# Kernel tuning notes

Hardware: AMD Instinct MI355X
Metric: run time of the kernel (lower is better)

Reference implementation:

```python
import jax, jax.numpy as jnp
import numpy as np

B, NS, NT, C = 32, 1000, 100, 256
LAMBDA_GIOU, LAMBDA_L1 = 10.0, 1.0


def _lsa(cost):
    """Hungarian / Jonker-Volgenant shortest-augmenting-path (numpy, O(n^2 m)).
    Matches scipy.optimize.linear_sum_assignment for rectangular matrices."""
    cost = np.asarray(cost, dtype=np.float64)
    transposed = cost.shape[0] > cost.shape[1]
    if transposed:
        cost = cost.T
    n, m = cost.shape  # n <= m
    INF = np.inf
    u = np.zeros(n + 1)
    v = np.zeros(m + 1)
    p = np.zeros(m + 1, dtype=np.int64)   # p[j] = row (1-based) assigned to col j
    way = np.zeros(m + 1, dtype=np.int64)
    for i in range(1, n + 1):
        p[0] = i
        j0 = 0
        minv = np.full(m + 1, INF)
        used = np.zeros(m + 1, dtype=bool)
        while True:
            used[j0] = True
            i0 = p[j0]
            cur = cost[i0 - 1, :] - u[i0] - v[1:]
            free = ~used[1:]
            better = free & (cur < minv[1:])
            minv[1:][better] = cur[better]
            way[1:][better] = j0
            masked = np.where(free, minv[1:], INF)
            j1 = int(np.argmin(masked)) + 1
            delta = masked[j1 - 1]
            u[p[used]] += delta
            v[used] -= delta
            minv[~used] -= delta
            j0 = j1
            if p[j0] == 0:
                break
        while j0:
            j1 = way[j0]
            p[j0] = p[j1]
            j0 = j1
    rows = p[1:] - 1
    cols = np.arange(m)
    keep = rows >= 0
    rows, cols = rows[keep], cols[keep]
    if transposed:
        rows, cols = cols, rows
    order = np.argsort(rows)
    return rows[order], cols[order]


def _pairwise_cost(logits, classes, sb, tb):
    """Per-batch (Ns,Nt) cost = CE(logits_s, class_t) + 10*(1-GIoU(box_s, box_t)) + L1mean."""
    Bc, Ns, Cd = logits.shape
    Nt = classes.shape[1]
    # Cross entropy: logsumexp over classes minus logit at target class (identical
    # math to the torch expand+flatten CE, without the Ns*Nt*C copy).
    lse = jax.nn.logsumexp(logits, axis=-1)  # (B,Ns)
    picked = jnp.take_along_axis(
        logits, jnp.broadcast_to(classes[:, None, :], (Bc, Ns, Nt)), axis=2)  # (B,Ns,Nt)
    ce = lse[:, :, None] - picked
    # Pairwise GIoU (boxes in xyxy)
    s = sb[:, :, None, :]  # (B,Ns,1,4)
    t = tb[:, None, :, :]  # (B,1,Nt,4)
    ix1 = jnp.maximum(s[..., 0], t[..., 0])
    iy1 = jnp.maximum(s[..., 1], t[..., 1])
    ix2 = jnp.minimum(s[..., 2], t[..., 2])
    iy2 = jnp.minimum(s[..., 3], t[..., 3])
    inter = jnp.clip(ix2 - ix1, 0.0) * jnp.clip(iy2 - iy1, 0.0)
    area_s = (s[..., 2] - s[..., 0]) * (s[..., 3] - s[..., 1])
    area_t = (t[..., 2] - t[..., 0]) * (t[..., 3] - t[..., 1])
    union = area_s + area_t - inter
    iou = inter / union
    cx1 = jnp.minimum(s[..., 0], t[..., 0])
    cy1 = jnp.minimum(s[..., 1], t[..., 1])
    cx2 = jnp.maximum(s[..., 2], t[..., 2])
    cy2 = jnp.maximum(s[..., 3], t[..., 3])
    carea = (cx2 - cx1) * (cy2 - cy1)
    giou = iou - (carea - union) / carea
    l1 = jnp.abs(s - t).mean(axis=-1)  # (B,Ns,Nt)
    return ce + LAMBDA_GIOU * (1.0 - giou) + LAMBDA_L1 * l1


def _valid_boxes(key, b, n):
    p = jax.random.uniform(key, (b, n, 2, 2), dtype=jnp.float32)
    lo = p.min(axis=2)
    hi = p.max(axis=2)
    return jnp.concatenate([lo, hi], axis=-1)  # (b,n,4) xyxy, x1<x2, y1<y2


def setup_inputs() -> dict:
    key = jax.random.key(0)
    k1, k2, k3, k4 = jax.random.split(key, 4)
    return {
        "source_class_logits": jax.random.normal(k1, (B, NS, C), dtype=jnp.float32),
        "target_classes": jax.random.randint(k2, (B, NT), 0, C, dtype=jnp.int32),
        "source_boxes": _valid_boxes(k3, B, NS),
        "target_boxes": _valid_boxes(k4, B, NT),
    }


def reference(source_class_logits, target_classes, source_boxes, target_boxes):
    cost = _pairwise_cost(source_class_logits, target_classes, source_boxes, target_boxes)
    cost_np = np.asarray(cost)
    rows_l, cols_l = [], []
    for b in range(cost_np.shape[0]):  # assignment is inherently per-matrix / host-side
        r, c = _lsa(cost_np[b])
        rows_l.append(r)
        cols_l.append(c)
    rows = jnp.asarray(np.stack(rows_l))  # (B, min(Ns,Nt))
    cols = jnp.asarray(np.stack(cols_l))
    bidx = jnp.arange(cost.shape[0])[:, None]
    return cost[bidx, rows, cols].mean(axis=1)  # (B,)
```

## Files before the change

kernel.cpp:

```cpp
#include <hip/hip_runtime.h>
#include <math.h>

#define NSRC 1000
#define NTGT 100
#define NCLS 256
#define NB   32
#define NSP  1024
#define CHUNK 64
#define NCHK  16
#define CEP   101
#define PAD_IDX(j) ((j) + ((j) >> 4))
#define LDSN (NSP + (NSP >> 4))
#define AUCTION_EPS 0.04f
#define NWAVES 8
#define ROUND_CAP 96


__global__ __launch_bounds__(512) void cost_kernel(const float* __restrict__ logits,
                                                   const int*   __restrict__ tcls,
                                                   const float* __restrict__ sbox,
                                                   const float* __restrict__ tbox,
                                                   float*       __restrict__ cost,
                                                   float*       __restrict__ pm1,
                                                   float*       __restrict__ pm2,
                                                   int*         __restrict__ pmi) {
    int b     = blockIdx.x & 31;
    int chunk = blockIdx.x >> 5;
    int s0    = chunk * CHUNK;
    int wid   = threadIdx.x >> 6;
    int lane  = threadIdx.x & 63;

    __shared__ float  ce_lds[CHUNK][CEP];
    __shared__ float4 sb_lds[CHUNK];
    __shared__ float4 tb_lds[NTGT];
    __shared__ int    cls_lds[128];

    for (int t = threadIdx.x; t < NTGT; t += 512) {
        tb_lds[t]  = reinterpret_cast<const float4*>(tbox)[b * NTGT + t];
        cls_lds[t] = tcls[b * NTGT + t];
    }
    if (threadIdx.x < 128 - NTGT) cls_lds[NTGT + threadIdx.x] = 0;
    int valid = NSRC - s0; valid = valid > CHUNK ? CHUNK : valid;
    for (int r = threadIdx.x; r < valid; r += 512)
        sb_lds[r] = reinterpret_cast<const float4*>(sbox)[b * NSRC + s0 + r];
    __syncthreads();

    int c0 = cls_lds[lane];
    int l0 = c0 >> 2, e0 = c0 & 3;
    int c1 = cls_lds[64 + lane];
    int l1s = c1 >> 2, e1 = c1 & 3;
    bool w1 = lane < NTGT - 64;
    #pragma unroll 4
    for (int r = wid; r < valid; r += 8) {
        int gs = b * NSRC + s0 + r;
        float4 v4 = reinterpret_cast<const float4*>(logits + (size_t)gs * NCLS)[lane];
        float m = fmaxf(fmaxf(v4.x, v4.y), fmaxf(v4.z, v4.w));
        #pragma unroll
        for (int off = 32; off >= 1; off >>= 1) m = fmaxf(m, __shfl_xor(m, off));
        float s = expf(v4.x - m) + expf(v4.y - m) + expf(v4.z - m) + expf(v4.w - m);
        #pragma unroll
        for (int off = 32; off >= 1; off >>= 1) s += __shfl_xor(s, off);
        float lse = m + logf(s);
        float px = __shfl(v4.x, l0), py = __shfl(v4.y, l0),
              pz = __shfl(v4.z, l0), pw = __shfl(v4.w, l0);
        float p0 = e0 == 0 ? px : e0 == 1 ? py : e0 == 2 ? pz : pw;
        ce_lds[r][lane] = lse - p0;
        float qx = __shfl(v4.x, l1s), qy = __shfl(v4.y, l1s),
              qz = __shfl(v4.z, l1s), qw = __shfl(v4.w, l1s);
        float p1 = e1 == 0 ? qx : e1 == 1 ? qy : e1 == 2 ? qz : qw;
        if (w1) ce_lds[r][64 + lane] = lse - p1;
    }
    __syncthreads();

    bool vs = lane < valid;
    float4 sb = sb_lds[vs ? lane : 0];
    float area_s = (sb.z - sb.x) * (sb.w - sb.y);
    int sg = s0 + lane;
    #pragma unroll 2
    for (int t = wid; t < NTGT; t += 8) {
        float4 tb = tb_lds[t];
        float area_t = (tb.z - tb.x) * (tb.w - tb.y);
        float c = 1e30f;
        if (vs) {
            float ce = ce_lds[lane][t];
            float ix1 = fmaxf(sb.x, tb.x), iy1 = fmaxf(sb.y, tb.y);
            float ix2 = fminf(sb.z, tb.z), iy2 = fminf(sb.w, tb.w);
            float inter = fmaxf(ix2 - ix1, 0.f) * fmaxf(iy2 - iy1, 0.f);
            float uni = area_s + area_t - inter;
            float iou = inter / uni;
            float cx1 = fminf(sb.x, tb.x), cy1 = fminf(sb.y, tb.y);
            float cx2 = fmaxf(sb.z, tb.z), cy2 = fmaxf(sb.w, tb.w);
            float carea = (cx2 - cx1) * (cy2 - cy1);
            float giou = iou - (carea - uni) / carea;
            float l1 = 0.25f * (fabsf(sb.x - tb.x) + fabsf(sb.y - tb.y) +
                                fabsf(sb.z - tb.z) + fabsf(sb.w - tb.w));
            c = ce + 10.0f * (1.0f - giou) + l1;
        }
        cost[(size_t)(b * NTGT + t) * NSP + sg] = c;
        float m1 = vs ? c : 1e38f, m2 = 1e38f;
        int   mi = vs ? sg : 0x7fffffff;
        #pragma unroll
        for (int off = 32; off >= 1; off >>= 1) {
            float om1 = __shfl_xor(m1, off);
            float om2 = __shfl_xor(m2, off);
            int   oi  = __shfl_xor(mi, off);
            bool take = (om1 < m1) || (om1 == m1 && oi < mi);
            float lose = take ? m1 : om1;
            m1 = take ? om1 : m1;
            mi = take ? oi  : mi;
            m2 = fminf(fminf(m2, om2), lose);
        }
        if (lane == 0) {
            int idx = (b * NTGT + t) * NCHK + chunk;
            pm1[idx] = m1; pm2[idx] = m2; pmi[idx] = mi;
        }
    }
}

__global__ __launch_bounds__(512) void lsa_kernel(const float* __restrict__ cost,
                                                  const float* __restrict__ pm1,
                                                  const float* __restrict__ pm2,
                                                  const int*   __restrict__ pmi,
                                                  float* __restrict__ out) {
    int b    = blockIdx.x;
    int tid  = threadIdx.x;
    int wv   = tid >> 6;
    int lane = tid & 63;
    const float* C = cost + (size_t)b * NTGT * NSP;
    __shared__ int   way[LDSN];
    __shared__ int   pcol[LDSN];
    __shared__ float uu[LDSN];
    __shared__ float vsh[LDSN];
    __shared__ float urow[NTGT];
    __shared__ int   done[NTGT];
    __shared__ float bm1[NTGT];
    __shared__ float bm2[NTGT];
    __shared__ int   bj [NTGT];
    __shared__ float bv [NTGT];
    __shared__ int   qbuf[1024];
    __shared__ int   qstate[2];
    __shared__ int   srow[NWAVES];

    for (int t = tid; t < LDSN; t += 512) {
        pcol[t] = -1; uu[t] = 0.f; vsh[t] = 0.f; way[t] = 0x7fffffff;
    }
    for (int t = tid; t < NTGT; t += 512) {
        int base16 = (b * NTGT + t) * NCHK;
        float m1 = pm1[base16], m2 = pm2[base16];
        int   mi = pmi[base16];
        #pragma unroll
        for (int k = 1; k < NCHK; ++k) {
            float om1 = pm1[base16 + k], om2 = pm2[base16 + k];
            int   oi  = pmi[base16 + k];
            bool take = (om1 < m1) || (om1 == m1 && oi < mi);
            float lose = take ? m1 : om1;
            m1 = take ? om1 : m1;
            mi = take ? oi  : mi;
            m2 = fminf(fminf(m2, om2), lose);
        }
        urow[t] = m1;
        bm1[t]  = m1;
        bm2[t]  = m2;
        bj[t]   = mi;
        bv[t]   = 0.f;
    }
    if (tid == 0) { qstate[0] = 0; qstate[1] = 0; }
    __syncthreads();

    for (int r = tid; r < NTGT; r += 512) atomicMin(&way[PAD_IDX(bj[r])], r);
    __syncthreads();
    for (int r = tid; r < NTGT; r += 512) {
        int j = bj[r];
        int w = (way[PAD_IDX(j)] == r) ? 1 : 0;
        done[r] = w;
        if (w) { pcol[PAD_IDX(j)] = r; uu[PAD_IDX(j)] = urow[r]; }
    }
    __syncthreads();

    if (tid < 64) {
        int qt = 0;
        #pragma unroll
        for (int r0 = 0; r0 < 128; r0 += 64) {
            int r = r0 + lane;
            bool act = (r < NTGT) && !done[r];
            unsigned long long mask = __ballot(act);
            if (act) qbuf[qt + __popcll(mask & ((1ull << lane) - 1ull))] = r;
            qt += __popcll(mask);
        }
        if (lane == 0) qstate[1] = qt;
    }
    __syncthreads();

    int base = lane * 16;

    for (int round = 0; round < ROUND_CAP; ++round) {
        int qh = qstate[0], qt = qstate[1];
        int navail = qt - qh;
        if (navail <= 0) break;
        int take = navail < NWAVES ? navail : NWAVES;
        if (wv < take) {
            int i = qbuf[(qh + wv) & 1023];
            if (lane == 0) srow[wv] = i;
            float m1p = bm1[i] + (bv[i] - vsh[PAD_IDX(bj[i])]);
            if (m1p > bm2[i]) {
                const float4* row4 = reinterpret_cast<const float4*>(C + (size_t)i * NSP + base);
                float m1 = 1e38f, m2 = 1e38f; int j1 = 0x7fffffff;
                #pragma unroll
                for (int q = 0; q < 4; ++q) {
                    float4 c4 = row4[q];
                    float vals[4];
                    vals[0] = c4.x - vsh[PAD_IDX(base + 4*q + 0)];
                    vals[1] = c4.y - vsh[PAD_IDX(base + 4*q + 1)];
                    vals[2] = c4.z - vsh[PAD_IDX(base + 4*q + 2)];
                    vals[3] = c4.w - vsh[PAD_IDX(base + 4*q + 3)];
                    #pragma unroll
                    for (int e = 0; e < 4; ++e) {
                        float val = vals[e];
                        if (val < m1) { m2 = m1; m1 = val; j1 = base + 4*q + e; }
                        else m2 = fminf(m2, val);
                    }
                }
                #pragma unroll
                for (int off = 32; off >= 1; off >>= 1) {
                    float om1 = __shfl_xor(m1, off);
                    float om2 = __shfl_xor(m2, off);
                    int   oj1 = __shfl_xor(j1, off);
                    bool tk = (om1 < m1) || (om1 == m1 && oj1 < j1);
                    float lose = tk ? m1 : om1;
                    m1 = tk ? om1 : m1;
                    j1 = tk ? oj1 : j1;
                    m2 = fminf(fminf(m2, om2), lose);
                }
                if (lane == 0) {
                    bm1[i] = m1; bm2[i] = m2; bj[i] = j1;
                    bv[i]  = vsh[PAD_IDX(j1)];
                }
            }
        }
        __syncthreads();
        if (tid == 0) {
            int qt2 = qstate[1];
            for (int s = 0; s < take; ++s) {
                int i  = srow[s];
                int j1 = bj[i];
                int pj1 = PAD_IDX(j1);
                float vnow = vsh[pj1];
                float m1p  = bm1[i] + (bv[i] - vnow);
                if (m1p <= bm2[i]) {
                    float delta = fmaxf(bm2[i] - m1p, AUCTION_EPS);
                    int old = pcol[pj1];
                    vsh[pj1]  = vnow - delta;
                    pcol[pj1] = i;
                    uu[pj1]   = m1p + delta;
                    urow[i]   = m1p + delta;
                    done[i]   = 1;
                    if (old >= 0) { qbuf[qt2 & 1023] = old; ++qt2; done[old] = 0; }
                } else {
                    qbuf[qt2 & 1023] = i; ++qt2;
                }
            }
            qstate[0] = qstate[0] + take;
            qstate[1] = qt2;
        }
        __syncthreads();
    }

    float v[16], d[16];
    if (tid < 64) {
        #pragma unroll
        for (int k = 0; k < 16; ++k) v[k] = vsh[PAD_IDX(base + k)];
    }
    __syncthreads();

    for (int i = 0; i < NTGT; ++i) {
        if (done[i]) continue;
        float ui = urow[i];
        float Df = 0.f;
        int jf = -1;
        if (tid < 64) {
            const float4* row4 = reinterpret_cast<const float4*>(C + (size_t)i * NSP + base);
            #pragma unroll
            for (int q = 0; q < 4; ++q) {
                float4 c4 = row4[q];
                d[4*q+0] = c4.x - ui - v[4*q+0];
                d[4*q+1] = c4.y - ui - v[4*q+1];
                d[4*q+2] = c4.z - ui - v[4*q+2];
                d[4*q+3] = c4.w - ui - v[4*q+3];
            }
            #pragma unroll
            for (int k = 0; k < 16; ++k) way[PAD_IDX(base + k)] = -1;
            unsigned int used = 0;
            int   pf_j = -1;
            float pfr[16];

            for (int it = 0; it < NTGT + 3; ++it) {
                float l1 = 1e38f, l2 = 1e38f;
                int   i1 = 0x7fffffff, i2 = 0x7fffffff;
                #pragma unroll
                for (int k = 0; k < 16; ++k) {
                    float val = ((used >> k) & 1u) ? 1e38f : d[k];
                    int idx = base + k;
                    if (val < l1) { l2 = l1; i2 = i1; l1 = val; i1 = idx; }
                    else if (val < l2) { l2 = val; i2 = idx; }
                }
                #pragma unroll
                for (int off = 32; off >= 1; off >>= 1) {
                    float ob1 = __shfl_xor(l1, off), ob2 = __shfl_xor(l2, off);
                    int   oc1 = __shfl_xor(i1, off), oc2 = __shfl_xor(i2, off);
                    bool tk = (ob1 < l1) || (ob1 == l1 && oc1 < i1);
                    float n1 = tk ? ob1 : l1; int ni1 = tk ? oc1 : i1;
                    float lz = tk ? l1  : ob1; int liz = tk ? i1  : oc1;
                    float n2 = lz; int ni2 = liz;
                    if (l2  < n2) { n2 = l2;  ni2 = i2;  }
                    if (ob2 < n2) { n2 = ob2; ni2 = oc2; }
                    l1 = n1; i1 = ni1; l2 = n2; i2 = ni2;
                }
                float wmin = l1; int j0 = i1; int j0b = i2;
                if (wmin >= 1e37f) break;
                int pj0 = pcol[PAD_IDX(j0)];
                if (pj0 < 0) { Df = wmin; jf = j0; break; }
                if ((j0 >> 4) == lane) used |= 1u << (j0 & 15);
                float uref = uu[PAD_IDX(j0)];
                float sft  = wmin - uref;
                float cr[16];
                if (pf_j == j0) {
                    #pragma unroll
                    for (int k = 0; k < 16; ++k) cr[k] = pfr[k];
                    pf_j = -1;
                } else {
                    const float4* rr = reinterpret_cast<const float4*>(C + (size_t)pj0 * NSP + base);
                    #pragma unroll
                    for (int q = 0; q < 4; ++q) {
                        float4 c4 = rr[q];
                        cr[4*q+0] = c4.x; cr[4*q+1] = c4.y; cr[4*q+2] = c4.z; cr[4*q+3] = c4.w;
                    }
                }
                if (j0b < NSP && j0b != pf_j) {
                    int pj0b = pcol[PAD_IDX(j0b)];
                    if (pj0b >= 0) {
                        const float4* rb = reinterpret_cast<const float4*>(C + (size_t)pj0b * NSP + base);
                        #pragma unroll
                        for (int q = 0; q < 4; ++q) {
                            float4 c4 = rb[q];
                            pfr[4*q+0] = c4.x; pfr[4*q+1] = c4.y;
                            pfr[4*q+2] = c4.z; pfr[4*q+3] = c4.w;
                        }
                        pf_j = j0b;
                    } else pf_j = -1;
                }
                #pragma unroll
                for (int k = 0; k < 16; ++k) {
                    float cand = sft + cr[k] - v[k];
                    bool upd = (cand < d[k]) && !((used >> k) & 1u);
                    if (upd) { d[k] = cand; way[PAD_IDX(base + k)] = j0; }
                }
            }

            if (jf >= 0) {
                #pragma unroll
                for (int k = 0; k < 16; ++k) {
                    if ((used >> k) & 1u) {
                        float diff = Df - d[k];
                        v[k] -= diff;
                        uu[PAD_IDX(base + k)] += diff;
                    }
                }
            }
        }
        __syncthreads();
        if (tid == 0 && jf >= 0) {
            int j = jf;
            for (int g = 0; g < NSP; ++g) {
                int jp = way[PAD_IDX(j)];
                if (jp < 0) { pcol[PAD_IDX(j)] = i; uu[PAD_IDX(j)] = ui + Df; break; }
                pcol[PAD_IDX(j)] = pcol[PAD_IDX(jp)];
                uu[PAD_IDX(j)]   = uu[PAD_IDX(jp)];
                j = jp;
            }
            done[i] = 1;
        }
        __syncthreads();
    }

    if (tid < 64) {
        float acc = 0.f;
        #pragma unroll
        for (int k = 0; k < 16; ++k) {
            int j = base + k;
            if (j < NSRC) {
                int r = pcol[PAD_IDX(j)];
                if (r >= 0) acc += C[(size_t)r * NSP + j];
            }
        }
        #pragma unroll
        for (int off = 32; off >= 1; off >>= 1) acc += __shfl_xor(acc, off);
        if (lane == 0) out[b] = acc * (1.0f / NTGT);
    }
}

extern "C" void kernel_launch(void* const* d_in, const int* in_sizes, int n_in,
                              void* d_out, int out_size, void* d_ws, size_t ws_size,
                              hipStream_t stream) {
    const float* logits = (const float*)d_in[0];
    const int*   tcls   = (const int*)  d_in[1];
    const float* sbox   = (const float*)d_in[2];
    const float* tbox   = (const float*)d_in[3];
    float* out = (float*)d_out;

    float* cost = (float*)d_ws;
    float* pm1  = cost + (size_t)NB * NTGT * NSP;
    float* pm2  = pm1 + (size_t)NB * NTGT * NCHK;
    int*   pmi  = (int*)(pm2 + (size_t)NB * NTGT * NCHK);

    cost_kernel<<<NB * NCHK, 512, 0, stream>>>(logits, tcls, sbox, tbox, cost,
                                               pm1, pm2, pmi);
    lsa_kernel <<<NB,        512, 0, stream>>>(cost, pm1, pm2, pmi, out);
}
```

Before: 124.8 us.

## Fuse cost and assignment kernels into one persistent kernel with atomic arrival barrier

Merges the cost-matrix kernel and the per-batch assignment kernel into a single launch. Each chunk block signals completion on a per-batch atomic counter, and the chunk-0 block for that batch spins until all chunks arrive before running the assignment. This removes the kernel boundary and launch gap but adds a memset launch. It also relies on all 512 blocks being co-resident, which launch_bounds(512,4) is meant to help with. The larger combined LDS footprint could reduce occupancy.

After: 135.3 us. +8.5%, slower.

```diff
diff --git a/kernel.cpp b/kernel.cpp
--- a/kernel.cpp
+++ b/kernel.cpp
@@ -16,117 +16,28 @@
 #define ROUND_CAP 96
 
 
-__global__ __launch_bounds__(512) void cost_kernel(const float* __restrict__ logits,
-                                                   const int*   __restrict__ tcls,
-                                                   const float* __restrict__ sbox,
-                                                   const float* __restrict__ tbox,
-                                                   float*       __restrict__ cost,
-                                                   float*       __restrict__ pm1,
-                                                   float*       __restrict__ pm2,
-                                                   int*         __restrict__ pmi) {
+__global__ __launch_bounds__(512, 4) void mega_kernel(
+        const float* __restrict__ logits,
+        const int*   __restrict__ tcls,
+        const float* __restrict__ sbox,
+        const float* __restrict__ tbox,
+        float*       __restrict__ cost,
+        float*       __restrict__ pm1,
+        float*       __restrict__ pm2,
+        int*         __restrict__ pmi,
+        int*         __restrict__ arrival,
+        float*       __restrict__ out) {
     int b     = blockIdx.x & 31;
     int chunk = blockIdx.x >> 5;
     int s0    = chunk * CHUNK;
-    int wid   = threadIdx.x >> 6;
-    int lane  = threadIdx.x & 63;
+    int tid   = threadIdx.x;
+    int wid   = tid >> 6;
+    int lane  = tid & 63;
 
     __shared__ float  ce_lds[CHUNK][CEP];
     __shared__ float4 sb_lds[CHUNK];
     __shared__ float4 tb_lds[NTGT];
     __shared__ int    cls_lds[128];
-
-    for (int t = threadIdx.x; t < NTGT; t += 512) {
-        tb_lds[t]  = reinterpret_cast<const float4*>(tbox)[b * NTGT + t];
-        cls_lds[t] = tcls[b * NTGT + t];
-    }
-    if (threadIdx.x < 128 - NTGT) cls_lds[NTGT + threadIdx.x] = 0;
-    int valid = NSRC - s0; valid = valid > CHUNK ? CHUNK : valid;
-    for (int r = threadIdx.x; r < valid; r += 512)
-        sb_lds[r] = reinterpret_cast<const float4*>(sbox)[b * NSRC + s0 + r];
-    __syncthreads();
-
-    int c0 = cls_lds[lane];
-    int l0 = c0 >> 2, e0 = c0 & 3;
-    int c1 = cls_lds[64 + lane];
-    int l1s = c1 >> 2, e1 = c1 & 3;
-    bool w1 = lane < NTGT - 64;
-    #pragma unroll 4
-    for (int r = wid; r < valid; r += 8) {
-        int gs = b * NSRC + s0 + r;
-        float4 v4 = reinterpret_cast<const float4*>(logits + (size_t)gs * NCLS)[lane];
-        float m = fmaxf(fmaxf(v4.x, v4.y), fmaxf(v4.z, v4.w));
-        #pragma unroll
-        for (int off = 32; off >= 1; off >>= 1) m = fmaxf(m, __shfl_xor(m, off));
-        float s = expf(v4.x - m) + expf(v4.y - m) + expf(v4.z - m) + expf(v4.w - m);
-        #pragma unroll
-        for (int off = 32; off >= 1; off >>= 1) s += __shfl_xor(s, off);
-        float lse = m + logf(s);
-        float px = __shfl(v4.x, l0), py = __shfl(v4.y, l0),
-              pz = __shfl(v4.z, l0), pw = __shfl(v4.w, l0);
-        float p0 = e0 == 0 ? px : e0 == 1 ? py : e0 == 2 ? pz : pw;
-        ce_lds[r][lane] = lse - p0;
-        float qx = __shfl(v4.x, l1s), qy = __shfl(v4.y, l1s),
-              qz = __shfl(v4.z, l1s), qw = __shfl(v4.w, l1s);
-        float p1 = e1 == 0 ? qx : e1 == 1 ? qy : e1 == 2 ? qz : qw;
-        if (w1) ce_lds[r][64 + lane] = lse - p1;
-    }
-    __syncthreads();
-
-    bool vs = lane < valid;
-    float4 sb = sb_lds[vs ? lane : 0];
-    float area_s = (sb.z - sb.x) * (sb.w - sb.y);
-    int sg = s0 + lane;
-    #pragma unroll 2
-    for (int t = wid; t < NTGT; t += 8) {
-        float4 tb = tb_lds[t];
-        float area_t = (tb.z - tb.x) * (tb.w - tb.y);
-        float c = 1e30f;
-        if (vs) {
-            float ce = ce_lds[lane][t];
-            float ix1 = fmaxf(sb.x, tb.x), iy1 = fmaxf(sb.y, tb.y);
-            float ix2 = fminf(sb.z, tb.z), iy2 = fminf(sb.w, tb.w);
-            float inter = fmaxf(ix2 - ix1, 0.f) * fmaxf(iy2 - iy1, 0.f);
-            float uni = area_s + area_t - inter;
-            float iou = inter / uni;
-            float cx1 = fminf(sb.x, tb.x), cy1 = fminf(sb.y, tb.y);
-            float cx2 = fmaxf(sb.z, tb.z), cy2 = fmaxf(sb.w, tb.w);
-            float carea = (cx2 - cx1) * (cy2 - cy1);
-            float giou = iou - (carea - uni) / carea;
-            float l1 = 0.25f * (fabsf(sb.x - tb.x) + fabsf(sb.y - tb.y) +
-                                fabsf(sb.z - tb.z) + fabsf(sb.w - tb.w));
-            c = ce + 10.0f * (1.0f - giou) + l1;
-        }
-        cost[(size_t)(b * NTGT + t) * NSP + sg] = c;
-        float m1 = vs ? c : 1e38f, m2 = 1e38f;
-        int   mi = vs ? sg : 0x7fffffff;
-        #pragma unroll
-        for (int off = 32; off >= 1; off >>= 1) {
-            float om1 = __shfl_xor(m1, off);
-            float om2 = __shfl_xor(m2, off);
-            int   oi  = __shfl_xor(mi, off);
-            bool take = (om1 < m1) || (om1 == m1 && oi < mi);
-            float lose = take ? m1 : om1;
-            m1 = take ? om1 : m1;
-            mi = take ? oi  : mi;
-            m2 = fminf(fminf(m2, om2), lose);
-        }
-        if (lane == 0) {
-            int idx = (b * NTGT + t) * NCHK + chunk;
-            pm1[idx] = m1; pm2[idx] = m2; pmi[idx] = mi;
-        }
-    }
-}
-
-__global__ __launch_bounds__(512) void lsa_kernel(const float* __restrict__ cost,
-                                                  const float* __restrict__ pm1,
-                                                  const float* __restrict__ pm2,
-                                                  const int*   __restrict__ pmi,
-                                                  float* __restrict__ out) {
-    int b    = blockIdx.x;
-    int tid  = threadIdx.x;
-    int wv   = tid >> 6;
-    int lane = tid & 63;
-    const float* C = cost + (size_t)b * NTGT * NSP;
     __shared__ int   way[LDSN];
     __shared__ int   pcol[LDSN];
     __shared__ float uu[LDSN];
@@ -141,9 +52,109 @@
     __shared__ int   qstate[2];
     __shared__ int   srow[NWAVES];
 
+    for (int t = tid; t < NTGT; t += 512) {
+        tb_lds[t]  = reinterpret_cast<const float4*>(tbox)[b * NTGT + t];
+        cls_lds[t] = tcls[b * NTGT + t];
+    }
+    if (tid < 128 - NTGT) cls_lds[NTGT + tid] = 0;
+    int valid = NSRC - s0; valid = valid > CHUNK ? CHUNK : valid;
+    for (int r = tid; r < valid; r += 512)
+        sb_lds[r] = reinterpret_cast<const float4*>(sbox)[b * NSRC + s0 + r];
+    __syncthreads();
+
+    int c0 = cls_lds[lane];
+    int l0 = c0 >> 2, e0 = c0 & 3;
+    int c1 = cls_lds[64 + lane];
+    int l1s = c1 >> 2, e1 = c1 & 3;
+    bool w1 = lane < NTGT - 64;
+    #pragma unroll 4
+    for (int r = wid; r < valid; r += 8) {
+        int gs = b * NSRC + s0 + r;
+        float4 v4 = reinterpret_cast<const float4*>(logits + (size_t)gs * NCLS)[lane];
+        float m = fmaxf(fmaxf(v4.x, v4.y), fmaxf(v4.z, v4.w));
+        #pragma unroll
+        for (int off = 32; off >= 1; off >>= 1) m = fmaxf(m, __shfl_xor(m, off));
+        float s = expf(v4.x - m) + expf(v4.y - m) + expf(v4.z - m) + expf(v4.w - m);
+        #pragma unroll
+        for (int off = 32; off >= 1; off >>= 1) s += __shfl_xor(s, off);
+        float lse = m + logf(s);
+        float px = __shfl(v4.x, l0), py = __shfl(v4.y, l0),
+              pz = __shfl(v4.z, l0), pw = __shfl(v4.w, l0);
+        float p0 = e0 == 0 ? px : e0 == 1 ? py : e0 == 2 ? pz : pw;
+        ce_lds[r][lane] = lse - p0;
+        float qx = __shfl(v4.x, l1s), qy = __shfl(v4.y, l1s),
+              qz = __shfl(v4.z, l1s), qw = __shfl(v4.w, l1s);
+        float p1 = e1 == 0 ? qx : e1 == 1 ? qy : e1 == 2 ? qz : qw;
+        if (w1) ce_lds[r][64 + lane] = lse - p1;
+    }
+    __syncthreads();
+
+    {
+        bool vs = lane < valid;
+        float4 sb = sb_lds[vs ? lane : 0];
+        float area_s = (sb.z - sb.x) * (sb.w - sb.y);
+        int sg = s0 + lane;
+        #pragma unroll 2
+        for (int t = wid; t < NTGT; t += 8) {
+            float4 tb = tb_lds[t];
+            float area_t = (tb.z - tb.x) * (tb.w - tb.y);
+            float c = 1e30f;
+            if (vs) {
+                float ce = ce_lds[lane][t];
+                float ix1 = fmaxf(sb.x, tb.x), iy1 = fmaxf(sb.y, tb.y);
+                float ix2 = fminf(sb.z, tb.z), iy2 = fminf(sb.w, tb.w);
+                float inter = fmaxf(ix2 - ix1, 0.f) * fmaxf(iy2 - iy1, 0.f);
+                float uni = area_s + area_t - inter;
+                float iou = inter / uni;
+                float cx1 = fminf(sb.x, tb.x), cy1 = fminf(sb.y, tb.y);
+                float cx2 = fmaxf(sb.z, tb.z), cy2 = fmaxf(sb.w, tb.w);
+                float carea = (cx2 - cx1) * (cy2 - cy1);
+                float giou = iou - (carea - uni) / carea;
+                float l1 = 0.25f * (fabsf(sb.x - tb.x) + fabsf(sb.y - tb.y) +
+                                    fabsf(sb.z - tb.z) + fabsf(sb.w - tb.w));
+                c = ce + 10.0f * (1.0f - giou) + l1;
+            }
+            cost[(size_t)(b * NTGT + t) * NSP + sg] = c;
+            float m1 = vs ? c : 1e38f, m2 = 1e38f;
+            int   mi = vs ? sg : 0x7fffffff;
+            #pragma unroll
+            for (int off = 32; off >= 1; off >>= 1) {
+                float om1 = __shfl_xor(m1, off);
+                float om2 = __shfl_xor(m2, off);
+                int   oi  = __shfl_xor(mi, off);
+                bool take = (om1 < m1) || (om1 == m1 && oi < mi);
+                float lose = take ? m1 : om1;
+                m1 = take ? om1 : m1;
+                mi = take ? oi  : mi;
+                m2 = fminf(fminf(m2, om2), lose);
+            }
+            if (lane == 0) {
+                int idx = (b * NTGT + t) * NCHK + chunk;
+                pm1[idx] = m1; pm2[idx] = m2; pmi[idx] = mi;
+            }
+        }
+    }
+
+    __syncthreads();
+    if (tid == 0)
+        __hip_atomic_fetch_add(&arrival[b * 16], 1, __ATOMIC_RELEASE,
+                               __HIP_MEMORY_SCOPE_AGENT);
+    if (chunk != 0) return;
+
+    int wv = wid;
+    const float* C = cost + (size_t)b * NTGT * NSP;
+
     for (int t = tid; t < LDSN; t += 512) {
         pcol[t] = -1; uu[t] = 0.f; vsh[t] = 0.f; way[t] = 0x7fffffff;
     }
+    if (tid == 0) {
+        while (__hip_atomic_load(&arrival[b * 16], __ATOMIC_ACQUIRE,
+                                 __HIP_MEMORY_SCOPE_AGENT) < NCHK) {
+            __builtin_amdgcn_s_sleep(1);
+        }
+    }
+    __syncthreads();
+
     for (int t = tid; t < NTGT; t += 512) {
         int base16 = (b * NTGT + t) * NCHK;
         float m1 = pm1[base16], m2 = pm2[base16];
@@ -411,8 +422,9 @@
     float* pm1  = cost + (size_t)NB * NTGT * NSP;
     float* pm2  = pm1 + (size_t)NB * NTGT * NCHK;
     int*   pmi  = (int*)(pm2 + (size_t)NB * NTGT * NCHK);
-
-    cost_kernel<<<NB * NCHK, 512, 0, stream>>>(logits, tcls, sbox, tbox, cost,
-                                               pm1, pm2, pmi);
-    lsa_kernel <<<NB,        512, 0, stream>>>(cost, pm1, pm2, pmi, out);
+    int*   arrival = pmi + (size_t)NB * NTGT * NCHK;
+
+    hipMemsetAsync(arrival, 0, NB * 16 * sizeof(int), stream);
+    mega_kernel<<<NB * NCHK, 512, 0, stream>>>(logits, tcls, sbox, tbox, cost,
+                                               pm1, pm2, pmi, arrival, out);
 }
```
